# Performance work log

Measured on AMD Instinct MI355X. Metric: run time of the kernel, lower is better.

## Reference

```python
import jax, jax.numpy as jnp
import numpy as np

EPSILON = 0.05
MAX_ITER = 50


def setup_inputs() -> dict:
    key = jax.random.key(0)
    k1, k2, k3 = jax.random.split(key, 3)
    B, N, M = 16, 2048, 2048
    cost = jax.random.uniform(k1, (B, N, M), dtype=jnp.float32)  # non-negative cost
    source_marginal = jax.random.uniform(k2, (B, N), dtype=jnp.float32)
    target_marginal = jax.random.uniform(k3, (B, M), dtype=jnp.float32)
    return {"cost": cost, "source_marginal": source_marginal, "target_marginal": target_marginal}


def reference(cost, source_marginal, target_marginal):
    # Log-domain Sinkhorn: fixed MAX_ITER iterations of dual updates.
    log_r = jnp.log(source_marginal + 1e-12)  # [B, N]
    log_c = jnp.log(target_marginal + 1e-12)  # [B, M]
    log_K = -cost / EPSILON                    # [B, N, M]

    log_u0 = jnp.zeros_like(log_r)
    log_v0 = jnp.zeros_like(log_c)

    def body(carry, _):
        log_u, log_v = carry
        log_u = log_r - jax.nn.logsumexp(log_K + log_v[:, None, :], axis=-1)
        log_v = log_c - jax.nn.logsumexp(log_K + log_u[:, :, None], axis=-2)
        return (log_u, log_v), None

    (log_u, log_v), _ = jax.lax.scan(body, (log_u0, log_v0), None, length=MAX_ITER)
    # Transport plan T = exp(log_u + log_K + log_v)
    return jnp.exp(log_u[:, :, None] + log_K + log_v[:, None, :])
```

## Files before the change

kernel.cpp:

```cpp
#include <hip/hip_runtime.h>
#include <cstdint>
#include <cstddef>

constexpr int B = 16, N = 2048, M = 2048;
constexpr int MAX_ITER = 50;
#define C2 (-28.853900817779268f)

constexpr int CHUNKS = 64;
constexpr int ROWS_PER_CHUNK = N / CHUNKS;
constexpr int ROWS_WG = 16;

__device__ __forceinline__ unsigned short f2bf(float f) {
  union { float f; unsigned u; } x; x.f = f;
  unsigned r = x.u + 0x7fffu + ((x.u >> 16) & 1u);
  return (unsigned short)(r >> 16);
}
__device__ __forceinline__ float bflo(unsigned w) { union { unsigned u; float f; } x; x.u = w << 16; return x.f; }
__device__ __forceinline__ float bfhi(unsigned w) { union { unsigned u; float f; } x; x.u = w & 0xffff0000u; return x.f; }

__global__ __launch_bounds__(256) void init_K(const float* __restrict__ cost,
                                              uint4* __restrict__ K,
                                              float* __restrict__ v) {
  unsigned gid = blockIdx.x * 256u + threadIdx.x;
  const float4* c4 = (const float4*)cost;
  float4 a = c4[(size_t)gid * 2];
  float4 b = c4[(size_t)gid * 2 + 1];
  float k0 = exp2f(a.x * C2), k1 = exp2f(a.y * C2), k2 = exp2f(a.z * C2), k3 = exp2f(a.w * C2);
  float k4 = exp2f(b.x * C2), k5 = exp2f(b.y * C2), k6 = exp2f(b.z * C2), k7 = exp2f(b.w * C2);
  uint4 w;
  w.x = (unsigned)f2bf(k0) | ((unsigned)f2bf(k1) << 16);
  w.y = (unsigned)f2bf(k2) | ((unsigned)f2bf(k3) << 16);
  w.z = (unsigned)f2bf(k4) | ((unsigned)f2bf(k5) << 16);
  w.w = (unsigned)f2bf(k6) | ((unsigned)f2bf(k7) << 16);
  K[gid] = w;
  if (gid < (unsigned)(B * M)) v[gid] = 1.0f;
}

__global__ __launch_bounds__(256) void init_v_only(float* __restrict__ v) {
  unsigned g = blockIdx.x * 256u + threadIdx.x;
  if (g < (unsigned)(B * M)) v[g] = 1.0f;
}

template <bool BF16K>
__global__ __launch_bounds__(256) void u_pass(const void* __restrict__ Kv_,
                                              const float* __restrict__ cost,
                                              const float* __restrict__ r,
                                              const float* __restrict__ v,
                                              float* __restrict__ u) {
  const int b = blockIdx.y;
  const int row0 = blockIdx.x * ROWS_WG;
  const int t = threadIdx.x;
  __shared__ float vs[M];
  const float4* vv = (const float4*)(v + (size_t)b * M);
  ((float4*)vs)[t]       = vv[t];
  ((float4*)vs)[t + 256] = vv[t + 256];
  __syncthreads();
  const int wave = t >> 6, lane = t & 63;
  float vreg[32];
#pragma unroll
  for (int it = 0; it < 4; ++it) {
    float4 a = ((const float4*)vs)[it * 128 + lane * 2];
    float4 c = ((const float4*)vs)[it * 128 + lane * 2 + 1];
    vreg[it * 8 + 0] = a.x; vreg[it * 8 + 1] = a.y; vreg[it * 8 + 2] = a.z; vreg[it * 8 + 3] = a.w;
    vreg[it * 8 + 4] = c.x; vreg[it * 8 + 5] = c.y; vreg[it * 8 + 6] = c.z; vreg[it * 8 + 7] = c.w;
  }
#pragma unroll
  for (int rr = 0; rr < ROWS_WG / 4; ++rr) {
    const int row = row0 + wave * (ROWS_WG / 4) + rr;
    float acc = 0.f;
    if (BF16K) {
      const uint4* Kr = (const uint4*)Kv_ + (size_t)(b * N + row) * (M / 8);
#pragma unroll
      for (int it = 0; it < 4; ++it) {
        uint4 w = Kr[it * 64 + lane];
        acc += bflo(w.x) * vreg[it * 8 + 0] + bfhi(w.x) * vreg[it * 8 + 1]
             + bflo(w.y) * vreg[it * 8 + 2] + bfhi(w.y) * vreg[it * 8 + 3]
             + bflo(w.z) * vreg[it * 8 + 4] + bfhi(w.z) * vreg[it * 8 + 5]
             + bflo(w.w) * vreg[it * 8 + 6] + bfhi(w.w) * vreg[it * 8 + 7];
      }
    } else {
      const float4* Cr = (const float4*)(cost + (size_t)(b * N + row) * M);
#pragma unroll
      for (int it = 0; it < 4; ++it) {
        float4 a = Cr[it * 128 + lane * 2];
        float4 c = Cr[it * 128 + lane * 2 + 1];
        acc += exp2f(a.x * C2) * vreg[it * 8 + 0] + exp2f(a.y * C2) * vreg[it * 8 + 1]
             + exp2f(a.z * C2) * vreg[it * 8 + 2] + exp2f(a.w * C2) * vreg[it * 8 + 3]
             + exp2f(c.x * C2) * vreg[it * 8 + 4] + exp2f(c.y * C2) * vreg[it * 8 + 5]
             + exp2f(c.z * C2) * vreg[it * 8 + 6] + exp2f(c.w * C2) * vreg[it * 8 + 7];
      }
    }
#pragma unroll
    for (int off = 32; off; off >>= 1) acc += __shfl_xor(acc, off, 64);
    if (lane == 0) u[b * N + row] = (r[b * N + row] + 1e-12f) / acc;
  }
}

template <bool BF16K>
__global__ __launch_bounds__(256) void col_pass(const void* __restrict__ Kv_,
                                                const float* __restrict__ cost,
                                                const float* __restrict__ u,
                                                float* __restrict__ part) {
  const int b = blockIdx.y, chunk = blockIdx.x;
  const int n0 = chunk * ROWS_PER_CHUNK;
  const int t = threadIdx.x;
  __shared__ float us[ROWS_PER_CHUNK];
  if (t < ROWS_PER_CHUNK) us[t] = u[b * N + n0 + t];
  __syncthreads();
  float acc[8] = {0, 0, 0, 0, 0, 0, 0, 0};
  if (BF16K) {
    const uint4* Kb = (const uint4*)Kv_ + (size_t)(b * N + n0) * (M / 8) + t;
#pragma unroll 4
    for (int n = 0; n < ROWS_PER_CHUNK; ++n) {
      uint4 w = Kb[(size_t)n * (M / 8)];
      float uval = us[n];
      acc[0] += bflo(w.x) * uval; acc[1] += bfhi(w.x) * uval;
      acc[2] += bflo(w.y) * uval; acc[3] += bfhi(w.y) * uval;
      acc[4] += bflo(w.z) * uval; acc[5] += bfhi(w.z) * uval;
      acc[6] += bflo(w.w) * uval; acc[7] += bfhi(w.w) * uval;
    }
  } else {
    const float4* Cb = (const float4*)(cost + (size_t)(b * N + n0) * M) + t * 2;
#pragma unroll 2
    for (int n = 0; n < ROWS_PER_CHUNK; ++n) {
      float4 a = Cb[(size_t)n * (M / 4)];
      float4 c = Cb[(size_t)n * (M / 4) + 1];
      float uval = us[n];
      acc[0] += exp2f(a.x * C2) * uval; acc[1] += exp2f(a.y * C2) * uval;
      acc[2] += exp2f(a.z * C2) * uval; acc[3] += exp2f(a.w * C2) * uval;
      acc[4] += exp2f(c.x * C2) * uval; acc[5] += exp2f(c.y * C2) * uval;
      acc[6] += exp2f(c.z * C2) * uval; acc[7] += exp2f(c.w * C2) * uval;
    }
  }
  float4* P = (float4*)(part + (size_t)(b * CHUNKS + chunk) * M) + t * 2;
  float4 o0; o0.x = acc[0]; o0.y = acc[1]; o0.z = acc[2]; o0.w = acc[3];
  float4 o1; o1.x = acc[4]; o1.y = acc[5]; o1.z = acc[6]; o1.w = acc[7];
  P[0] = o0; P[1] = o1;
}

__global__ __launch_bounds__(256) void v_fin(const float* __restrict__ part,
                                             const float* __restrict__ c,
                                             float* __restrict__ v) {
  const int g = blockIdx.x * 256 + threadIdx.x;
  const int b = g >> 11, m = g & (M - 1);
  float s = 0.f;
#pragma unroll 8
  for (int ch = 0; ch < CHUNKS; ++ch) s += part[(size_t)(b * CHUNKS + ch) * M + m];
  v[g] = (c[g] + 1e-12f) / s;
}

__global__ __launch_bounds__(256) void final_T(const float* __restrict__ cost,
                                               const float* __restrict__ u,
                                               const float* __restrict__ v,
                                               float* __restrict__ out) {
  const int b = blockIdx.z, n = blockIdx.y;
  const int m4 = blockIdx.x * 256 + threadIdx.x;
  const float un = u[b * N + n];
  float4 vv = ((const float4*)(v + (size_t)b * M))[m4];
  const size_t off = ((size_t)(b * N + n) * M) / 4 + m4;
  float4 cc = ((const float4*)cost)[off];
  float4 o;
  o.x = un * vv.x * exp2f(cc.x * C2);
  o.y = un * vv.y * exp2f(cc.y * C2);
  o.z = un * vv.z * exp2f(cc.z * C2);
  o.w = un * vv.w * exp2f(cc.w * C2);
  ((float4*)out)[off] = o;
}

extern "C" void kernel_launch(void* const* d_in, const int* in_sizes, int n_in,
                              void* d_out, int out_size, void* d_ws, size_t ws_size,
                              hipStream_t stream) {
  const float* cost = (const float*)d_in[0];
  const float* r    = (const float*)d_in[1];
  const float* c    = (const float*)d_in[2];
  float* out        = (float*)d_out;
  char* ws          = (char*)d_ws;

  const size_t K_bytes    = (size_t)B * N * M * 2;
  const size_t u_bytes    = (size_t)B * N * 4;
  const size_t v_bytes    = (size_t)B * M * 4;
  const size_t part_bytes = (size_t)B * CHUNKS * M * 4;
  const size_t need_main  = K_bytes + u_bytes + v_bytes + part_bytes;
  const bool useK = (ws_size >= need_main);

  void* K; float *u, *v, *part;
  if (useK) {
    K = ws;
    u = (float*)(ws + K_bytes);
  } else {
    K = nullptr;
    u = (float*)ws;
  }
  v = u + (size_t)B * N;
  part = v + (size_t)B * M;

  if (useK) {
    init_K<<<dim3((B * (size_t)N * M) / (256 * 8)), 256, 0, stream>>>(cost, (uint4*)K, v);
  } else {
    init_v_only<<<dim3((B * M + 255) / 256), 256, 0, stream>>>(v);
  }

  for (int it = 0; it < MAX_ITER; ++it) {
    if (useK) {
      u_pass<true><<<dim3(N / ROWS_WG, B), 256, 0, stream>>>(K, cost, r, v, u);
      col_pass<true><<<dim3(CHUNKS, B), 256, 0, stream>>>(K, cost, u, part);
    } else {
      u_pass<false><<<dim3(N / ROWS_WG, B), 256, 0, stream>>>(nullptr, cost, r, v, u);
      col_pass<false><<<dim3(CHUNKS, B), 256, 0, stream>>>(nullptr, cost, u, part);
    }
    v_fin<<<dim3(B * M / 256), 256, 0, stream>>>(part, c, v);
  }

  final_T<<<dim3(M / 1024, N, B), 256, 0, stream>>>(cost, u, v, out);
}
```

Before: 2.851 ms.

## Fuse row and column passes into one kernel per chunk to reuse K

Merges the u (row) pass and the column partial-sum pass into a single kernel, where each workgroup handles a 32-row chunk: it computes u for its rows, keeps them in shared memory, and immediately does the column accumulation over the same K rows. The second read of the chunk can then hit cache instead of making a separate full pass over K, and one launch per iteration is removed. The first iteration initialises v to one inside the kernel, and init_K now does 16 elements per thread. In exchange, the u pass now runs on only 1024 workgroups of 8 rows per wave instead of 2048, which lowers parallelism for that phase.

Result: faster. 2.734 ms (-4.1%).

```diff
diff --git a/kernel.cpp b/kernel.cpp
--- a/kernel.cpp
+++ b/kernel.cpp
@@ -8,7 +8,6 @@
 
 constexpr int CHUNKS = 64;
 constexpr int ROWS_PER_CHUNK = N / CHUNKS;
-constexpr int ROWS_WG = 16;
 
 __device__ __forceinline__ unsigned short f2bf(float f) {
   union { float f; unsigned u; } x; x.f = f;
@@ -19,42 +18,53 @@
 __device__ __forceinline__ float bfhi(unsigned w) { union { unsigned u; float f; } x; x.u = w & 0xffff0000u; return x.f; }
 
 __global__ __launch_bounds__(256) void init_K(const float* __restrict__ cost,
-                                              uint4* __restrict__ K,
-                                              float* __restrict__ v) {
+                                              uint4* __restrict__ K) {
   unsigned gid = blockIdx.x * 256u + threadIdx.x;
   const float4* c4 = (const float4*)cost;
-  float4 a = c4[(size_t)gid * 2];
-  float4 b = c4[(size_t)gid * 2 + 1];
-  float k0 = exp2f(a.x * C2), k1 = exp2f(a.y * C2), k2 = exp2f(a.z * C2), k3 = exp2f(a.w * C2);
-  float k4 = exp2f(b.x * C2), k5 = exp2f(b.y * C2), k6 = exp2f(b.z * C2), k7 = exp2f(b.w * C2);
-  uint4 w;
-  w.x = (unsigned)f2bf(k0) | ((unsigned)f2bf(k1) << 16);
-  w.y = (unsigned)f2bf(k2) | ((unsigned)f2bf(k3) << 16);
-  w.z = (unsigned)f2bf(k4) | ((unsigned)f2bf(k5) << 16);
-  w.w = (unsigned)f2bf(k6) | ((unsigned)f2bf(k7) << 16);
-  K[gid] = w;
-  if (gid < (unsigned)(B * M)) v[gid] = 1.0f;
-}
-
-__global__ __launch_bounds__(256) void init_v_only(float* __restrict__ v) {
-  unsigned g = blockIdx.x * 256u + threadIdx.x;
-  if (g < (unsigned)(B * M)) v[g] = 1.0f;
-}
-
-template <bool BF16K>
-__global__ __launch_bounds__(256) void u_pass(const void* __restrict__ Kv_,
-                                              const float* __restrict__ cost,
-                                              const float* __restrict__ r,
-                                              const float* __restrict__ v,
-                                              float* __restrict__ u) {
-  const int b = blockIdx.y;
-  const int row0 = blockIdx.x * ROWS_WG;
+  uint4 w0, w1;
+  {
+    float4 a = c4[(size_t)gid * 4 + 0];
+    float4 b = c4[(size_t)gid * 4 + 1];
+    w0.x = (unsigned)f2bf(exp2f(a.x * C2)) | ((unsigned)f2bf(exp2f(a.y * C2)) << 16);
+    w0.y = (unsigned)f2bf(exp2f(a.z * C2)) | ((unsigned)f2bf(exp2f(a.w * C2)) << 16);
+    w0.z = (unsigned)f2bf(exp2f(b.x * C2)) | ((unsigned)f2bf(exp2f(b.y * C2)) << 16);
+    w0.w = (unsigned)f2bf(exp2f(b.z * C2)) | ((unsigned)f2bf(exp2f(b.w * C2)) << 16);
+  }
+  {
+    float4 a = c4[(size_t)gid * 4 + 2];
+    float4 b = c4[(size_t)gid * 4 + 3];
+    w1.x = (unsigned)f2bf(exp2f(a.x * C2)) | ((unsigned)f2bf(exp2f(a.y * C2)) << 16);
+    w1.y = (unsigned)f2bf(exp2f(a.z * C2)) | ((unsigned)f2bf(exp2f(a.w * C2)) << 16);
+    w1.z = (unsigned)f2bf(exp2f(b.x * C2)) | ((unsigned)f2bf(exp2f(b.y * C2)) << 16);
+    w1.w = (unsigned)f2bf(exp2f(b.z * C2)) | ((unsigned)f2bf(exp2f(b.w * C2)) << 16);
+  }
+  K[(size_t)gid * 2]     = w0;
+  K[(size_t)gid * 2 + 1] = w1;
+}
+
+template <bool FIRST>
+__global__ __launch_bounds__(256) void iter_fused(const uint4* __restrict__ K,
+                                                  const float* __restrict__ r,
+                                                  const float* __restrict__ v,
+                                                  float* __restrict__ u_out,
+                                                  float* __restrict__ part) {
+  const int b = blockIdx.y, chunk = blockIdx.x;
+  const int n0 = chunk * ROWS_PER_CHUNK;
   const int t = threadIdx.x;
   __shared__ float vs[M];
-  const float4* vv = (const float4*)(v + (size_t)b * M);
-  ((float4*)vs)[t]       = vv[t];
-  ((float4*)vs)[t + 256] = vv[t + 256];
-  __syncthreads();
+  __shared__ float us[ROWS_PER_CHUNK];
+
+  if (FIRST) {
+    float4 one; one.x = one.y = one.z = one.w = 1.0f;
+    ((float4*)vs)[t] = one;
+    ((float4*)vs)[t + 256] = one;
+  } else {
+    const float4* vv = (const float4*)(v + (size_t)b * M);
+    ((float4*)vs)[t]       = vv[t];
+    ((float4*)vs)[t + 256] = vv[t + 256];
+  }
+  __syncthreads();
+
   const int wave = t >> 6, lane = t & 63;
   float vreg[32];
 #pragma unroll
@@ -64,77 +74,45 @@
     vreg[it * 8 + 0] = a.x; vreg[it * 8 + 1] = a.y; vreg[it * 8 + 2] = a.z; vreg[it * 8 + 3] = a.w;
     vreg[it * 8 + 4] = c.x; vreg[it * 8 + 5] = c.y; vreg[it * 8 + 6] = c.z; vreg[it * 8 + 7] = c.w;
   }
-#pragma unroll
-  for (int rr = 0; rr < ROWS_WG / 4; ++rr) {
-    const int row = row0 + wave * (ROWS_WG / 4) + rr;
+
+#pragma unroll
+  for (int rr = 0; rr < ROWS_PER_CHUNK / 4; ++rr) {
+    const int lrow = wave * (ROWS_PER_CHUNK / 4) + rr;
+    const int row = n0 + lrow;
+    const uint4* Kr = K + (size_t)(b * N + row) * (M / 8);
     float acc = 0.f;
-    if (BF16K) {
-      const uint4* Kr = (const uint4*)Kv_ + (size_t)(b * N + row) * (M / 8);
-#pragma unroll
-      for (int it = 0; it < 4; ++it) {
-        uint4 w = Kr[it * 64 + lane];
-        acc += bflo(w.x) * vreg[it * 8 + 0] + bfhi(w.x) * vreg[it * 8 + 1]
-             + bflo(w.y) * vreg[it * 8 + 2] + bfhi(w.y) * vreg[it * 8 + 3]
-             + bflo(w.z) * vreg[it * 8 + 4] + bfhi(w.z) * vreg[it * 8 + 5]
-             + bflo(w.w) * vreg[it * 8 + 6] + bfhi(w.w) * vreg[it * 8 + 7];
-      }
-    } else {
-      const float4* Cr = (const float4*)(cost + (size_t)(b * N + row) * M);
-#pragma unroll
-      for (int it = 0; it < 4; ++it) {
-        float4 a = Cr[it * 128 + lane * 2];
-        float4 c = Cr[it * 128 + lane * 2 + 1];
-        acc += exp2f(a.x * C2) * vreg[it * 8 + 0] + exp2f(a.y * C2) * vreg[it * 8 + 1]
-             + exp2f(a.z * C2) * vreg[it * 8 + 2] + exp2f(a.w * C2) * vreg[it * 8 + 3]
-             + exp2f(c.x * C2) * vreg[it * 8 + 4] + exp2f(c.y * C2) * vreg[it * 8 + 5]
-             + exp2f(c.z * C2) * vreg[it * 8 + 6] + exp2f(c.w * C2) * vreg[it * 8 + 7];
-      }
+#pragma unroll
+    for (int it = 0; it < 4; ++it) {
+      uint4 w = Kr[it * 64 + lane];
+      acc += bflo(w.x) * vreg[it * 8 + 0] + bfhi(w.x) * vreg[it * 8 + 1]
+           + bflo(w.y) * vreg[it * 8 + 2] + bfhi(w.y) * vreg[it * 8 + 3]
+           + bflo(w.z) * vreg[it * 8 + 4] + bfhi(w.z) * vreg[it * 8 + 5]
+           + bflo(w.w) * vreg[it * 8 + 6] + bfhi(w.w) * vreg[it * 8 + 7];
     }
 #pragma unroll
     for (int off = 32; off; off >>= 1) acc += __shfl_xor(acc, off, 64);
-    if (lane == 0) u[b * N + row] = (r[b * N + row] + 1e-12f) / acc;
-  }
-}
-
-template <bool BF16K>
-__global__ __launch_bounds__(256) void col_pass(const void* __restrict__ Kv_,
-                                                const float* __restrict__ cost,
-                                                const float* __restrict__ u,
-                                                float* __restrict__ part) {
-  const int b = blockIdx.y, chunk = blockIdx.x;
-  const int n0 = chunk * ROWS_PER_CHUNK;
-  const int t = threadIdx.x;
-  __shared__ float us[ROWS_PER_CHUNK];
-  if (t < ROWS_PER_CHUNK) us[t] = u[b * N + n0 + t];
-  __syncthreads();
-  float acc[8] = {0, 0, 0, 0, 0, 0, 0, 0};
-  if (BF16K) {
-    const uint4* Kb = (const uint4*)Kv_ + (size_t)(b * N + n0) * (M / 8) + t;
-#pragma unroll 4
-    for (int n = 0; n < ROWS_PER_CHUNK; ++n) {
-      uint4 w = Kb[(size_t)n * (M / 8)];
-      float uval = us[n];
-      acc[0] += bflo(w.x) * uval; acc[1] += bfhi(w.x) * uval;
-      acc[2] += bflo(w.y) * uval; acc[3] += bfhi(w.y) * uval;
-      acc[4] += bflo(w.z) * uval; acc[5] += bfhi(w.z) * uval;
-      acc[6] += bflo(w.w) * uval; acc[7] += bfhi(w.w) * uval;
-    }
-  } else {
-    const float4* Cb = (const float4*)(cost + (size_t)(b * N + n0) * M) + t * 2;
-#pragma unroll 2
-    for (int n = 0; n < ROWS_PER_CHUNK; ++n) {
-      float4 a = Cb[(size_t)n * (M / 4)];
-      float4 c = Cb[(size_t)n * (M / 4) + 1];
-      float uval = us[n];
-      acc[0] += exp2f(a.x * C2) * uval; acc[1] += exp2f(a.y * C2) * uval;
-      acc[2] += exp2f(a.z * C2) * uval; acc[3] += exp2f(a.w * C2) * uval;
-      acc[4] += exp2f(c.x * C2) * uval; acc[5] += exp2f(c.y * C2) * uval;
-      acc[6] += exp2f(c.z * C2) * uval; acc[7] += exp2f(c.w * C2) * uval;
-    }
+    if (lane == 0) {
+      float uval = (r[b * N + row] + 1e-12f) / acc;
+      us[lrow] = uval;
+      u_out[b * N + row] = uval;
+    }
+  }
+  __syncthreads();
+
+  float acc8[8] = {0, 0, 0, 0, 0, 0, 0, 0};
+  const uint4* Kb = K + (size_t)(b * N + n0) * (M / 8) + t;
+#pragma unroll 8
+  for (int n = 0; n < ROWS_PER_CHUNK; ++n) {
+    uint4 w = Kb[(size_t)n * (M / 8)];
+    float uval = us[n];
+    acc8[0] += bflo(w.x) * uval; acc8[1] += bfhi(w.x) * uval;
+    acc8[2] += bflo(w.y) * uval; acc8[3] += bfhi(w.y) * uval;
+    acc8[4] += bflo(w.z) * uval; acc8[5] += bfhi(w.z) * uval;
+    acc8[6] += bflo(w.w) * uval; acc8[7] += bfhi(w.w) * uval;
   }
   float4* P = (float4*)(part + (size_t)(b * CHUNKS + chunk) * M) + t * 2;
-  float4 o0; o0.x = acc[0]; o0.y = acc[1]; o0.z = acc[2]; o0.w = acc[3];
-  float4 o1; o1.x = acc[4]; o1.y = acc[5]; o1.z = acc[6]; o1.w = acc[7];
+  float4 o0; o0.x = acc8[0]; o0.y = acc8[1]; o0.z = acc8[2]; o0.w = acc8[3];
+  float4 o1; o1.x = acc8[4]; o1.y = acc8[5]; o1.z = acc8[6]; o1.w = acc8[7];
   P[0] = o0; P[1] = o1;
 }
 
@@ -167,6 +145,81 @@
   ((float4*)out)[off] = o;
 }
 
+__global__ __launch_bounds__(256) void init_v_only(float* __restrict__ v) {
+  unsigned g = blockIdx.x * 256u + threadIdx.x;
+  if (g < (unsigned)(B * M)) v[g] = 1.0f;
+}
+
+template <bool FIRST>
+__global__ __launch_bounds__(256) void iter_fused_cost(const float* __restrict__ cost,
+                                                       const float* __restrict__ r,
+                                                       const float* __restrict__ v,
+                                                       float* __restrict__ u_out,
+                                                       float* __restrict__ part) {
+  const int b = blockIdx.y, chunk = blockIdx.x;
+  const int n0 = chunk * ROWS_PER_CHUNK;
+  const int t = threadIdx.x;
+  __shared__ float vs[M];
+  __shared__ float us[ROWS_PER_CHUNK];
+  if (FIRST) {
+    float4 one; one.x = one.y = one.z = one.w = 1.0f;
+    ((float4*)vs)[t] = one; ((float4*)vs)[t + 256] = one;
+  } else {
+    const float4* vv = (const float4*)(v + (size_t)b * M);
+    ((float4*)vs)[t] = vv[t]; ((float4*)vs)[t + 256] = vv[t + 256];
+  }
+  __syncthreads();
+  const int wave = t >> 6, lane = t & 63;
+  float vreg[32];
+#pragma unroll
+  for (int it = 0; it < 4; ++it) {
+    float4 a = ((const float4*)vs)[it * 128 + lane * 2];
+    float4 c = ((const float4*)vs)[it * 128 + lane * 2 + 1];
+    vreg[it * 8 + 0] = a.x; vreg[it * 8 + 1] = a.y; vreg[it * 8 + 2] = a.z; vreg[it * 8 + 3] = a.w;
+    vreg[it * 8 + 4] = c.x; vreg[it * 8 + 5] = c.y; vreg[it * 8 + 6] = c.z; vreg[it * 8 + 7] = c.w;
+  }
+#pragma unroll
+  for (int rr = 0; rr < ROWS_PER_CHUNK / 4; ++rr) {
+    const int lrow = wave * (ROWS_PER_CHUNK / 4) + rr;
+    const int row = n0 + lrow;
+    const float4* Cr = (const float4*)(cost + (size_t)(b * N + row) * M);
+    float acc = 0.f;
+#pragma unroll
+    for (int it = 0; it < 4; ++it) {
+      float4 a = Cr[it * 128 + lane * 2];
+      float4 c = Cr[it * 128 + lane * 2 + 1];
+      acc += exp2f(a.x * C2) * vreg[it * 8 + 0] + exp2f(a.y * C2) * vreg[it * 8 + 1]
+           + exp2f(a.z * C2) * vreg[it * 8 + 2] + exp2f(a.w * C2) * vreg[it * 8 + 3]
+           + exp2f(c.x * C2) * vreg[it * 8 + 4] + exp2f(c.y * C2) * vreg[it * 8 + 5]
+           + exp2f(c.z * C2) * vreg[it * 8 + 6] + exp2f(c.w * C2) * vreg[it * 8 + 7];
+    }
+#pragma unroll
+    for (int off = 32; off; off >>= 1) acc += __shfl_xor(acc, off, 64);
+    if (lane == 0) {
+      float uval = (r[b * N + row] + 1e-12f) / acc;
+      us[lrow] = uval;
+      u_out[b * N + row] = uval;
+    }
+  }
+  __syncthreads();
+  float acc8[8] = {0, 0, 0, 0, 0, 0, 0, 0};
+  const float4* Cb = (const float4*)(cost + (size_t)(b * N + n0) * M) + t * 2;
+#pragma unroll 2
+  for (int n = 0; n < ROWS_PER_CHUNK; ++n) {
+    float4 a = Cb[(size_t)n * (M / 4)];
+    float4 c = Cb[(size_t)n * (M / 4) + 1];
+    float uval = us[n];
+    acc8[0] += exp2f(a.x * C2) * uval; acc8[1] += exp2f(a.y * C2) * uval;
+    acc8[2] += exp2f(a.z * C2) * uval; acc8[3] += exp2f(a.w * C2) * uval;
+    acc8[4] += exp2f(c.x * C2) * uval; acc8[5] += exp2f(c.y * C2) * uval;
+    acc8[6] += exp2f(c.z * C2) * uval; acc8[7] += exp2f(c.w * C2) * uval;
+  }
+  float4* P = (float4*)(part + (size_t)(b * CHUNKS + chunk) * M) + t * 2;
+  float4 o0; o0.x = acc8[0]; o0.y = acc8[1]; o0.z = acc8[2]; o0.w = acc8[3];
+  float4 o1; o1.x = acc8[4]; o1.y = acc8[5]; o1.z = acc8[6]; o1.w = acc8[7];
+  P[0] = o0; P[1] = o1;
+}
+
 extern "C" void kernel_launch(void* const* d_in, const int* in_sizes, int n_in,
                               void* d_out, int out_size, void* d_ws, size_t ws_size,
                               hipStream_t stream) {
@@ -183,9 +236,9 @@
   const size_t need_main  = K_bytes + u_bytes + v_bytes + part_bytes;
   const bool useK = (ws_size >= need_main);
 
-  void* K; float *u, *v, *part;
+  uint4* K; float *u, *v, *part;
   if (useK) {
-    K = ws;
+    K = (uint4*)ws;
     u = (float*)(ws + K_bytes);
   } else {
     K = nullptr;
@@ -195,20 +248,20 @@
   part = v + (size_t)B * M;
 
   if (useK) {
-    init_K<<<dim3((B * (size_t)N * M) / (256 * 8)), 256, 0, stream>>>(cost, (uint4*)K, v);
-  } else {
-    init_v_only<<<dim3((B * M + 255) / 256), 256, 0, stream>>>(v);
-  }
-
-  for (int it = 0; it < MAX_ITER; ++it) {
-    if (useK) {
-      u_pass<true><<<dim3(N / ROWS_WG, B), 256, 0, stream>>>(K, cost, r, v, u);
-      col_pass<true><<<dim3(CHUNKS, B), 256, 0, stream>>>(K, cost, u, part);
-    } else {
-      u_pass<false><<<dim3(N / ROWS_WG, B), 256, 0, stream>>>(nullptr, cost, r, v, u);
-      col_pass<false><<<dim3(CHUNKS, B), 256, 0, stream>>>(nullptr, cost, u, part);
-    }
+    init_K<<<dim3((B * (size_t)N * M) / (256 * 16)), 256, 0, stream>>>(cost, K);
+    iter_fused<true><<<dim3(CHUNKS, B), 256, 0, stream>>>(K, r, v, u, part);
     v_fin<<<dim3(B * M / 256), 256, 0, stream>>>(part, c, v);
+    for (int it = 1; it < MAX_ITER; ++it) {
+      iter_fused<false><<<dim3(CHUNKS, B), 256, 0, stream>>>(K, r, v, u, part);
+      v_fin<<<dim3(B * M / 256), 256, 0, stream>>>(part, c, v);
+    }
+  } else {
+    iter_fused_cost<true><<<dim3(CHUNKS, B), 256, 0, stream>>>(cost, r, v, u, part);
+    v_fin<<<dim3(B * M / 256), 256, 0, stream>>>(part, c, v);
+    for (int it = 1; it < MAX_ITER; ++it) {
+      iter_fused_cost<false><<<dim3(CHUNKS, B), 256, 0, stream>>>(cost, r, v, u, part);
+      v_fin<<<dim3(B * M / 256), 256, 0, stream>>>(part, c, v);
+    }
   }
 
   final_T<<<dim3(M / 1024, N, B), 256, 0, stream>>>(cost, u, v, out);
```
